# Kernel optimization log

Hardware: AMD Instinct MI355X
Metric: run time of the kernel (lower is better)

## Reference

```python
import jax, jax.numpy as jnp
import numpy as np

B, S, DM, H, HD = 2, 2048, 1024, 16, 64
MEM_SIZE = 1000
K_SIMILAR, K_CONTIG = 8, 2
K_TOTAL = K_SIMILAR + K_CONTIG  # 10 memory tokens
NEG = -1e9


def setup_inputs() -> dict:
    key = jax.random.key(0)
    k1, k2, k3, k4, k5, k6 = jax.random.split(key, 6)
    inputs = jax.random.normal(k1, (B, S, DM), dtype=jnp.float32)
    attention_mask = jnp.ones((B, S), dtype=jnp.float32)
    Wq = jax.random.normal(k2, (DM, H * HD), dtype=jnp.float32) * 0.02
    Wk = jax.random.normal(k3, (DM, H * HD), dtype=jnp.float32) * 0.02
    Wv = jax.random.normal(k4, (DM, H * HD), dtype=jnp.float32) * 0.02
    Wo = jax.random.normal(k5, (H * HD, DM), dtype=jnp.float32) * 0.02
    events = jax.random.normal(k6, (MEM_SIZE, H * HD), dtype=jnp.float32) * 0.02
    return {"inputs": inputs, "attention_mask": attention_mask,
            "Wq": Wq, "Wk": Wk, "Wv": Wv, "Wo": Wo, "events": events}


def _forward(inputs, attention_mask, Wq, Wk, Wv, Wo, events):
    # projections (no bias), split heads: [B, H, S, HD]
    q = (inputs @ Wq).reshape(B, S, H, HD).transpose(0, 2, 1, 3)
    k = (inputs @ Wk).reshape(B, S, H, HD).transpose(0, 2, 1, 3)
    v = (inputs @ Wv).reshape(B, S, H, HD).transpose(0, 2, 1, 3)

    # --- episodic retrieval: cosine top-k of last-token key vs events ---
    qvec = k[:, :, -1, :].reshape(B, H * HD)                       # [B, D]
    qn = qvec / (jnp.linalg.norm(qvec, axis=-1, keepdims=True) + 1e-8)
    en = events / (jnp.linalg.norm(events, axis=-1, keepdims=True) + 1e-8)
    sims = qn @ en.T                                               # [B, M]
    _, topk_idx = jax.lax.top_k(sims, K_TOTAL)                     # [B, K]
    retrieved = events[topk_idx]                                   # [B, K, D]
    retrieved_k = retrieved.reshape(B, K_TOTAL, H, HD).transpose(0, 2, 1, 3)  # [B,H,K,HD]
    retrieved_v = retrieved_k                                      # non-differential path

    aug_k = jnp.concatenate([retrieved_k, k], axis=2)              # [B,H,K+S,HD]
    aug_v = jnp.concatenate([retrieved_v, v], axis=2)

    # --- ALiBi bias: slopes * (pos_i - pos_j) on original cols, 0 on memory cols ---
    slopes = 2.0 ** (-8.0 * jnp.arange(1, H + 1, dtype=jnp.float32) / H)  # [H]
    positions = jnp.arange(S, dtype=jnp.float32)
    pos_diff = positions[:, None] - positions[None, :]             # [S, S]
    alibi = slopes[:, None, None] * pos_diff                       # [H, S, S]
    alibi = jnp.concatenate([jnp.zeros((H, S, K_TOTAL), jnp.float32), alibi], axis=-1)

    # --- causal mask: -1e9 strictly-upper on original cols, 0 on memory cols ---
    tri = jnp.where(jnp.arange(S)[None, :] > jnp.arange(S)[:, None], NEG, 0.0)  # [S,S]
    causal = jnp.concatenate([jnp.zeros((S, K_TOTAL), jnp.float32), tri], axis=-1)

    # --- padding mask: memory tokens always attendable ---
    aug_mask = jnp.concatenate([jnp.ones((B, K_TOTAL), jnp.float32), attention_mask], axis=-1)
    mask_bias = (1.0 - aug_mask)[:, None, None, :] * NEG           # [B,1,1,K+S]

    scores = jnp.einsum("bhqd,bhkd->bhqk", q, aug_k) / np.sqrt(HD)
    scores = scores + alibi[None] + causal[None, None] + mask_bias
    attn = jax.nn.softmax(scores, axis=-1)
    out = jnp.einsum("bhqk,bhkd->bhqd", attn, aug_v)               # [B,H,S,HD]
    out = out.transpose(0, 2, 1, 3).reshape(B, S, H * HD)
    return out @ Wo


def reference(inputs, attention_mask, Wq, Wk, Wv, Wo, events):
    return _forward(inputs, attention_mask, Wq, Wk, Wv, Wo, events)
```

## Files before the change

### kernel.cpp

```cpp
#include <hip/hip_runtime.h>
#include <hip/hip_bf16.h>
#include <math.h>

#define B_   2
#define S_   2048
#define DM_  1024
#define H_   16
#define HD_  64
#define MEM_ 1000
#define KTOT 10
#define NROW (B_ * S_)
#define NEG9 (-1e9f)
#define LDK  72

typedef __attribute__((ext_vector_type(8))) short short8;
typedef __attribute__((ext_vector_type(4))) float f32x4;

__device__ __forceinline__ void gll16(const __hip_bfloat16* g, __hip_bfloat16* l) {
    __builtin_amdgcn_global_load_lds(
        (const __attribute__((address_space(1))) void*)g,
        (__attribute__((address_space(3))) void*)l, 16, 0, 0);
}

__global__ __launch_bounds__(256) void convert_a(const float* __restrict__ in,
                                                 __hip_bfloat16* __restrict__ out) {
    const size_t i = ((size_t)blockIdx.x * 256 + threadIdx.x) * 8;
    float4 a = *(const float4*)&in[i];
    float4 b = *(const float4*)&in[i + 4];
    alignas(16) __hip_bfloat16 t[8];
    t[0] = __float2bfloat16(a.x); t[1] = __float2bfloat16(a.y);
    t[2] = __float2bfloat16(a.z); t[3] = __float2bfloat16(a.w);
    t[4] = __float2bfloat16(b.x); t[5] = __float2bfloat16(b.y);
    t[6] = __float2bfloat16(b.z); t[7] = __float2bfloat16(b.w);
    *(short8*)&out[i] = *(short8*)t;
}

__global__ __launch_bounds__(256) void convert_wT(const float* __restrict__ Wq,
                                                  const float* __restrict__ Wk,
                                                  const float* __restrict__ Wv,
                                                  const float* __restrict__ Wo,
                                                  __hip_bfloat16* __restrict__ Wt) {
    const int g = blockIdx.z;
    const float* W = (g == 0) ? Wq : (g == 1) ? Wk : (g == 2) ? Wv : Wo;
    const int n0 = blockIdx.x * 64, k0 = blockIdx.y * 64;
    __shared__ float T[64][65];
    const int tid = threadIdx.x;
    {
        const int r = tid >> 4, c4 = (tid & 15) * 4;
#pragma unroll
        for (int p = 0; p < 4; ++p) {
            float4 v = *(const float4*)&W[(size_t)(k0 + r + p * 16) * 1024 + n0 + c4];
            T[r + p * 16][c4 + 0] = v.x; T[r + p * 16][c4 + 1] = v.y;
            T[r + p * 16][c4 + 2] = v.z; T[r + p * 16][c4 + 3] = v.w;
        }
    }
    __syncthreads();
    {
        const int n = tid >> 3, off = (tid & 7) * 8;
#pragma unroll
        for (int p = 0; p < 2; ++p) {
            const int nn = n + p * 32;
            alignas(16) __hip_bfloat16 t[8];
#pragma unroll
            for (int j = 0; j < 8; ++j) t[j] = __float2bfloat16(T[off + j][nn]);
            *(short8*)&Wt[((size_t)(g * 1024 + n0 + nn)) * 1024 + k0 + off] = *(short8*)t;
        }
    }
}

__device__ __forceinline__ void store_out(__hip_bfloat16* p, float x) { *p = __float2bfloat16(x); }
__device__ __forceinline__ void store_out(float* p, float x) { *p = x; }

template <typename OutT>
__global__ __launch_bounds__(256) void gemm_mfma(const __hip_bfloat16* __restrict__ A,
                                                 const __hip_bfloat16* __restrict__ Bt,
                                                 OutT* __restrict__ C, int ldc) {
    __shared__ __hip_bfloat16 As[128 * 32];
    __shared__ __hip_bfloat16 Bs[128 * 32];
    const int tid = threadIdx.x;
    const int wave = tid >> 6, lane = tid & 63;
    const int quad = lane >> 4, lm = lane & 15;
    const int wr = wave >> 1, wc = wave & 1;
    const int m0 = blockIdx.y * 128, n0 = blockIdx.x * 128;

    const int r0 = tid >> 2, c0 = (tid & 3) * 8;
    const __hip_bfloat16* ga0 = &A[(size_t)(m0 + r0) * 1024 + c0];
    const __hip_bfloat16* ga1 = &A[(size_t)(m0 + 64 + r0) * 1024 + c0];
    const __hip_bfloat16* gb0 = &Bt[(size_t)(n0 + r0) * 1024 + c0];
    const __hip_bfloat16* gb1 = &Bt[(size_t)(n0 + 64 + r0) * 1024 + c0];
    __hip_bfloat16* la0 = &As[(wave * 64) * 8];
    __hip_bfloat16* la1 = &As[(256 + wave * 64) * 8];
    __hip_bfloat16* lb0 = &Bs[(wave * 64) * 8];
    __hip_bfloat16* lb1 = &Bs[(256 + wave * 64) * 8];

    f32x4 acc[4][4];
#pragma unroll
    for (int i = 0; i < 4; ++i)
#pragma unroll
        for (int j = 0; j < 4; ++j) acc[i][j] = (f32x4){0.f, 0.f, 0.f, 0.f};

    for (int k0 = 0; k0 < 1024; k0 += 32) {
        __syncthreads();
        gll16(ga0 + k0, la0);
        gll16(ga1 + k0, la1);
        gll16(gb0 + k0, lb0);
        gll16(gb1 + k0, lb1);
        __syncthreads();
        short8 af[4], bf4[4];
#pragma unroll
        for (int mt = 0; mt < 4; ++mt)
            af[mt] = *(const short8*)&As[(wr * 64 + mt * 16 + lm) * 32 + quad * 8];
#pragma unroll
        for (int nt = 0; nt < 4; ++nt)
            bf4[nt] = *(const short8*)&Bs[(wc * 64 + nt * 16 + lm) * 32 + quad * 8];
#pragma unroll
        for (int mt = 0; mt < 4; ++mt)
#pragma unroll
            for (int nt = 0; nt < 4; ++nt)
                acc[mt][nt] = __builtin_amdgcn_mfma_f32_16x16x32_bf16(
                    af[mt], bf4[nt], acc[mt][nt], 0, 0, 0);
    }
#pragma unroll
    for (int mt = 0; mt < 4; ++mt)
#pragma unroll
        for (int nt = 0; nt < 4; ++nt) {
            const int col = n0 + wc * 64 + nt * 16 + lm;
#pragma unroll
            for (int i = 0; i < 4; ++i) {
                const int row = m0 + wr * 64 + mt * 16 + quad * 4 + i;
                store_out(&C[(size_t)row * ldc + col], acc[mt][nt][i]);
            }
        }
}

__global__ __launch_bounds__(256) void lastk_kernel(const float* __restrict__ inputs,
                                                    const float* __restrict__ Wk,
                                                    float* __restrict__ lk) {
    const int b = blockIdx.y;
    const int cl = threadIdx.x & 63;
    const int col = blockIdx.x * 64 + cl;
    const int kq = threadIdx.x >> 6;
    __shared__ float xr[1024];
    __shared__ float part[4][64];
    for (int i = threadIdx.x; i < 1024; i += 256)
        xr[i] = inputs[((size_t)(b * S_ + S_ - 1)) * 1024 + i];
    __syncthreads();
    float acc = 0.f;
#pragma unroll 4
    for (int k = kq * 256; k < kq * 256 + 256; ++k)
        acc += xr[k] * Wk[(size_t)k * 1024 + col];
    part[kq][cl] = acc;
    __syncthreads();
    if (threadIdx.x < 64)
        lk[b * 1024 + blockIdx.x * 64 + threadIdx.x] =
            part[0][threadIdx.x] + part[1][threadIdx.x] +
            part[2][threadIdx.x] + part[3][threadIdx.x];
}

__global__ __launch_bounds__(256) void sims_kernel(const float* __restrict__ lk,
                                                   const float* __restrict__ events,
                                                   float* __restrict__ sims) {
    const int b = blockIdx.y;
    const int tid = threadIdx.x;
    const int wave = tid >> 6, lane = tid & 63;
    __shared__ float qv[1024];
    for (int i = tid; i < 1024; i += 256)
        qv[i] = lk[b * 1024 + i];
    __syncthreads();

    const int m = blockIdx.x * 4 + wave;
    if (m >= MEM_) return;
    const float* ev = &events[(size_t)m * 1024];
    float dot = 0.f, nrm = 0.f;
    for (int d = lane; d < 1024; d += 64) {
        float e = ev[d];
        dot += qv[d] * e;
        nrm += e * e;
    }
    for (int off = 32; off; off >>= 1) {
        dot += __shfl_down(dot, off);
        nrm += __shfl_down(nrm, off);
    }
    if (lane == 0) sims[b * 1024 + m] = dot / (sqrtf(nrm) + 1e-8f);
}

__global__ __launch_bounds__(256) void topk10_kernel(const float* __restrict__ sims,
                                                     int* __restrict__ topk) {
    const int b = blockIdx.x;
    const int tid = threadIdx.x;
    __shared__ float sv[1024];
    __shared__ float bv[256];
    __shared__ int   bi[256];
    for (int m = tid; m < 1024; m += 256)
        sv[m] = (m < MEM_) ? sims[b * 1024 + m] : -INFINITY;
    __syncthreads();

    for (int it = 0; it < KTOT; ++it) {
        float best = -INFINITY; int besti = 0x7fffffff;
        for (int m = tid; m < 1024; m += 256) {
            float s = sv[m];
            if (s > best || (s == best && m < besti)) { best = s; besti = m; }
        }
        bv[tid] = best; bi[tid] = besti;
        __syncthreads();
        for (int stride = 128; stride; stride >>= 1) {
            if (tid < stride) {
                float ov = bv[tid + stride]; int oi = bi[tid + stride];
                if (ov > bv[tid] || (ov == bv[tid] && oi < bi[tid])) {
                    bv[tid] = ov; bi[tid] = oi;
                }
            }
            __syncthreads();
        }
        if (tid == 0) { topk[b * KTOT + it] = bi[0]; sv[bi[0]] = -INFINITY; }
        __syncthreads();
    }
}

__global__ __launch_bounds__(256) void attn_mfma(
        const __hip_bfloat16* __restrict__ qkv,
        const float* __restrict__ events,
        const int* __restrict__ topk,
        const float* __restrict__ amask,
        __hip_bfloat16* __restrict__ out) {
    const int b = blockIdx.y >> 4, h = blockIdx.y & 15;
    const int qt = (blockIdx.x + blockIdx.y) & 31;
    const int q0 = qt * 64;
    const int tid = threadIdx.x;
    const int wave = tid >> 6, lane = tid & 63;
    const int quad = lane >> 4, lm = lane & 15;

    const __hip_bfloat16* qf = qkv;
    const __hip_bfloat16* kf = qkv + 1024;
    const __hip_bfloat16* vf = qkv + 2048;

    __shared__ __hip_bfloat16 Qs[64 * LDK];
    __shared__ __hip_bfloat16 Ks[64 * LDK];
    __shared__ __hip_bfloat16 Vt[64 * LDK];
    __shared__ __hip_bfloat16 Ps[64 * LDK];
    __shared__ float colb[64];
    __shared__ float redb[4];

    const float slope = exp2f(-0.5f * (float)(h + 1));

    const int va = tid & 31, vdc = tid >> 5;
    const int vtok0 = va * 2, vd0 = vdc * 8;

    {
        const __hip_bfloat16* src = &qf[((size_t)(b * S_ + q0)) * 3072 + h * 64];
#pragma unroll
        for (int u = 0; u < 2; ++u) {
            int c = tid * 2 + u, row = c >> 3, off = (c & 7) * 8;
            *(short8*)&Qs[row * LDK + off] =
                *(const short8*)&src[(size_t)row * 3072 + off];
        }
    }
    for (int i = tid * 8; i < 64 * LDK; i += 256 * 8)
        *(int4*)&Vt[i] = make_int4(0, 0, 0, 0);
    __syncthreads();
    if (tid < 80) {
        const int tok = tid >> 3, d0 = (tid & 7) * 8;
        const int ev = topk[b * KTOT + tok];
        const float* es = &events[(size_t)ev * 1024 + h * 64 + d0];
#pragma unroll
        for (int j = 0; j < 8; ++j) {
            __hip_bfloat16 x = __float2bfloat16(es[j]);
            Ks[tok * LDK + d0 + j] = x;
            Vt[(d0 + j) * LDK + tok] = x;
        }
    }
    __syncthreads();

    float m_[4], l_[4], mshift[4];
    f32x4 Oa[4];
#pragma unroll
    for (int i = 0; i < 4; ++i) {
        m_[i] = -INFINITY; l_[i] = 0.f;
        mshift[i] = -slope * (float)(q0 + wave * 16 + quad * 4 + i);
    }
#pragma unroll
    for (int nt = 0; nt < 4; ++nt) Oa[nt] = (f32x4){0.f, 0.f, 0.f, 0.f};

    short8 pk[2], pv0, pv1;
    float pam = 1.f;
    auto prefetchKV = [&](int kt) {
        const __hip_bfloat16* ks = &kf[((size_t)(b * S_ + kt * 64)) * 3072 + h * 64];
#pragma unroll
        for (int u = 0; u < 2; ++u) {
            int c = tid * 2 + u, row = c >> 3, off = (c & 7) * 8;
            pk[u] = *(const short8*)&ks[(size_t)row * 3072 + off];
        }
        const __hip_bfloat16* v0 =
            &vf[((size_t)(b * S_ + kt * 64 + vtok0)) * 3072 + h * 64 + vd0];
        pv0 = *(const short8*)v0;
        pv1 = *(const short8*)(v0 + 3072);
        if (tid < 64) pam = amask[b * S_ + kt * 64 + tid];
    };
    auto stageKV = [&](int kt) {
#pragma unroll
        for (int u = 0; u < 2; ++u) {
            int c = tid * 2 + u, row = c >> 3, off = (c & 7) * 8;
            *(short8*)&Ks[row * LDK + off] = pk[u];
        }
#pragma unroll
        for (int j = 0; j < 8; ++j) {
            short2 pr; pr.x = pv0[j]; pr.y = pv1[j];
            *(short2*)&Vt[(vd0 + j) * LDK + vtok0] = pr;
        }
        if (tid < 64)
            colb[tid] = fmaf(-slope, (float)(kt * 64 + tid), (1.f - pam) * NEG9);
    };

    auto qk = [&](f32x4* sa) {
#pragma unroll
        for (int nt = 0; nt < 4; ++nt) sa[nt] = (f32x4){0.f, 0.f, 0.f, 0.f};
#pragma unroll
        for (int ks2 = 0; ks2 < 2; ++ks2) {
            short8 aq = *(const short8*)&Qs[(wave * 16 + lm) * LDK + ks2 * 32 + quad * 8];
#pragma unroll
            for (int nt = 0; nt < 4; ++nt) {
                short8 bk = *(const short8*)&Ks[(nt * 16 + lm) * LDK + ks2 * 32 + quad * 8];
                sa[nt] = __builtin_amdgcn_mfma_f32_16x16x32_bf16(aq, bk, sa[nt], 0, 0, 0);
            }
        }
    };
    auto pv = [&]() {
#pragma unroll
        for (int ks2 = 0; ks2 < 2; ++ks2) {
            short8 ap = *(const short8*)&Ps[(wave * 16 + lm) * LDK + ks2 * 32 + quad * 8];
#pragma unroll
            for (int nt = 0; nt < 4; ++nt) {
                short8 bv = *(const short8*)&Vt[(nt * 16 + lm) * LDK + ks2 * 32 + quad * 8];
                Oa[nt] = __builtin_amdgcn_mfma_f32_16x16x32_bf16(ap, bv, Oa[nt], 0, 0, 0);
            }
        }
    };

    auto softmax_online = [&](const f32x4* sa, int kt, bool diag) {
        float cb[4];
        if (kt >= 0) {
#pragma unroll
            for (int nt = 0; nt < 4; ++nt) cb[nt] = colb[nt * 16 + lm];
        }
#pragma unroll
        for (int i = 0; i < 4; ++i) {
            const int lr = wave * 16 + quad * 4 + i;
            const int rg = q0 + lr;
            float s[4];
#pragma unroll
            for (int nt = 0; nt < 4; ++nt) {
                const int cc = nt * 16 + lm;
                if (kt < 0) {
                    s[nt] = (cc < KTOT) ? fmaf(sa[nt][i], 0.125f, mshift[i]) : NEG9;
                } else {
                    float v = fmaf(sa[nt][i], 0.125f, cb[nt]);
                    s[nt] = (diag && kt * 64 + cc > rg) ? NEG9 : v;
                }
            }
            float rmax = fmaxf(fmaxf(s[0], s[1]), fmaxf(s[2], s[3]));
#pragma unroll
            for (int off = 1; off < 16; off <<= 1)
                rmax = fmaxf(rmax, __shfl_xor(rmax, off, 16));
            const float newm = fmaxf(m_[i], rmax);
            const float al = __expf(m_[i] - newm);
            float p[4], ps = 0.f;
#pragma unroll
            for (int nt = 0; nt < 4; ++nt) {
                p[nt] = __expf(s[nt] - newm);
                ps += p[nt];
            }
#pragma unroll
            for (int off = 1; off < 16; off <<= 1)
                ps += __shfl_xor(ps, off, 16);
            l_[i] = l_[i] * al + ps;
            m_[i] = newm;
#pragma unroll
            for (int nt = 0; nt < 4; ++nt) {
                Oa[nt][i] *= al;
                Ps[lr * LDK + nt * 16 + lm] = __float2bfloat16(p[nt]);
            }
        }
    };

    auto softmax_fast = [&](const f32x4* sa, int cbase, bool diag) {
        float cb[4];
#pragma unroll
        for (int nt = 0; nt < 4; ++nt) cb[nt] = colb[nt * 16 + lm];
#pragma unroll
        for (int i = 0; i < 4; ++i) {
            const int lr = wave * 16 + quad * 4 + i;
            const float cm = m_[i];
            float p[4];
#pragma unroll
            for (int nt = 0; nt < 4; ++nt)
                p[nt] = __expf(fmaf(sa[nt][i], 0.125f, cb[nt]) - cm);
            if (diag) {
                const int rg = q0 + lr;
#pragma unroll
                for (int nt = 0; nt < 4; ++nt)
                    if (cbase + nt * 16 + lm > rg) p[nt] = 0.f;
            }
            float ps = (p[0] + p[1]) + (p[2] + p[3]);
#pragma unroll
            for (int off = 1; off < 16; off <<= 1)
                ps += __shfl_xor(ps, off, 16);
            l_[i] += ps;
#pragma unroll
            for (int nt = 0; nt < 4; ++nt)
                Ps[lr * LDK + nt * 16 + lm] = __float2bfloat16(p[nt]);
        }
    };

    prefetchKV(0);
    {
        f32x4 sa[4];
        qk(sa);
        softmax_online(sa, -1, false);
        pv();
    }
    __syncthreads();
    stageKV(0);
    if (qt >= 1) prefetchKV(1);
    __syncthreads();
    {
        f32x4 sa[4];
        qk(sa);
        softmax_online(sa, 0, qt == 0);
        pv();
    }

    int ktend = 0;
    if (qt >= 1) {
        float mloc = fminf(fminf(m_[0], m_[1]), fminf(m_[2], m_[3]));
#pragma unroll
        for (int off = 1; off < 64; off <<= 1)
            mloc = fminf(mloc, __shfl_xor(mloc, off, 64));
        if (lane == 0) redb[wave] = mloc;
        __syncthreads();
        const float mmin = fminf(fminf(redb[0], redb[1]), fminf(redb[2], redb[3]));
        ktend = min(qt, (int)((118.f - mmin) / (64.f * slope)));
    }
    for (int kt = 1; kt <= ktend; ++kt) {
        __syncthreads();
        stageKV(kt);
        if (kt < ktend) prefetchKV(kt + 1);
        __syncthreads();
        f32x4 sa[4];
        qk(sa);
        softmax_fast(sa, kt * 64, kt == qt);
        pv();
    }

#pragma unroll
    for (int i = 0; i < 4; ++i) {
        const int lr = wave * 16 + quad * 4 + i;
        const float inv = 1.f / l_[i];
        __hip_bfloat16* dst = &out[((size_t)(b * S_ + q0 + lr)) * 1024 + h * 64 + lm];
#pragma unroll
        for (int nt = 0; nt < 4; ++nt)
            dst[nt * 16] = __float2bfloat16(Oa[nt][i] * inv);
    }
}

extern "C" void kernel_launch(void* const* d_in, const int* in_sizes, int n_in,
                              void* d_out, int out_size, void* d_ws, size_t ws_size,
                              hipStream_t stream) {
    const float* inputs = (const float*)d_in[0];
    const float* amask  = (const float*)d_in[1];
    const float* Wq     = (const float*)d_in[2];
    const float* Wk     = (const float*)d_in[3];
    const float* Wv     = (const float*)d_in[4];
    const float* Wo     = (const float*)d_in[5];
    const float* events = (const float*)d_in[6];
    float* out = (float*)d_out;

    __hip_bfloat16* Ax  = (__hip_bfloat16*)d_ws;
    __hip_bfloat16* Wt  = Ax + (size_t)NROW * 1024;
    __hip_bfloat16* qkv = Wt + (size_t)4096 * 1024;
    __hip_bfloat16* ao  = qkv + (size_t)NROW * 3072;
    float* lk   = (float*)(ao + (size_t)NROW * 1024);
    float* sims = lk + 2 * 1024;
    int* topk   = (int*)(sims + 2 * 1024);

    dim3 blk(256);
    convert_a<<<2048, blk, 0, stream>>>(inputs, Ax);
    convert_wT<<<dim3(16, 16, 4), blk, 0, stream>>>(Wq, Wk, Wv, Wo, Wt);
    gemm_mfma<__hip_bfloat16><<<dim3(24, 32), blk, 0, stream>>>(Ax, Wt, qkv, 3072);
    lastk_kernel<<<dim3(16, B_), blk, 0, stream>>>(inputs, Wk, lk);
    sims_kernel<<<dim3(250, B_), blk, 0, stream>>>(lk, events, sims);
    topk10_kernel<<<B_, 256, 0, stream>>>(sims, topk);
    attn_mfma<<<dim3(32, 32), blk, 0, stream>>>(qkv, events, topk, amask, ao);
    gemm_mfma<float><<<dim3(8, 32), blk, 0, stream>>>(
        ao, Wt + (size_t)3072 * 1024, out, 1024);
}
```

Baseline: 269.9 us.

## Merge prep kernels and make attention persistent with atomic work queue

```diff
diff --git a/kernel.cpp b/kernel.cpp
--- a/kernel.cpp
+++ b/kernel.cpp
@@ -12,6 +12,7 @@
 #define NROW (B_ * S_)
 #define NEG9 (-1e9f)
 #define LDK  72
+#define NITEMS 1024
 
 typedef __attribute__((ext_vector_type(8))) short short8;
 typedef __attribute__((ext_vector_type(4))) float f32x4;
@@ -22,49 +23,79 @@
         (__attribute__((address_space(3))) void*)l, 16, 0, 0);
 }
 
-__global__ __launch_bounds__(256) void convert_a(const float* __restrict__ in,
-                                                 __hip_bfloat16* __restrict__ out) {
-    const size_t i = ((size_t)blockIdx.x * 256 + threadIdx.x) * 8;
-    float4 a = *(const float4*)&in[i];
-    float4 b = *(const float4*)&in[i + 4];
-    alignas(16) __hip_bfloat16 t[8];
-    t[0] = __float2bfloat16(a.x); t[1] = __float2bfloat16(a.y);
-    t[2] = __float2bfloat16(a.z); t[3] = __float2bfloat16(a.w);
-    t[4] = __float2bfloat16(b.x); t[5] = __float2bfloat16(b.y);
-    t[6] = __float2bfloat16(b.z); t[7] = __float2bfloat16(b.w);
-    *(short8*)&out[i] = *(short8*)t;
-}
-
-__global__ __launch_bounds__(256) void convert_wT(const float* __restrict__ Wq,
-                                                  const float* __restrict__ Wk,
-                                                  const float* __restrict__ Wv,
-                                                  const float* __restrict__ Wo,
-                                                  __hip_bfloat16* __restrict__ Wt) {
-    const int g = blockIdx.z;
-    const float* W = (g == 0) ? Wq : (g == 1) ? Wk : (g == 2) ? Wv : Wo;
-    const int n0 = blockIdx.x * 64, k0 = blockIdx.y * 64;
-    __shared__ float T[64][65];
-    const int tid = threadIdx.x;
+__global__ __launch_bounds__(256) void prep(const float* __restrict__ inputs,
+                                            const float* __restrict__ Wq,
+                                            const float* __restrict__ Wk,
+                                            const float* __restrict__ Wv,
+                                            const float* __restrict__ Wo,
+                                            __hip_bfloat16* __restrict__ Ax,
+                                            __hip_bfloat16* __restrict__ Wt,
+                                            float* __restrict__ lk,
+                                            int* __restrict__ ctr) {
+    const int bx = blockIdx.x, tid = threadIdx.x;
+    if (bx == 0 && tid == 0) *ctr = 0;
+
+    if (bx < 2048) {
+        const size_t i = ((size_t)bx * 256 + tid) * 8;
+        float4 a = *(const float4*)&inputs[i];
+        float4 b = *(const float4*)&inputs[i + 4];
+        alignas(16) __hip_bfloat16 t[8];
+        t[0] = __float2bfloat16(a.x); t[1] = __float2bfloat16(a.y);
+        t[2] = __float2bfloat16(a.z); t[3] = __float2bfloat16(a.w);
+        t[4] = __float2bfloat16(b.x); t[5] = __float2bfloat16(b.y);
+        t[6] = __float2bfloat16(b.z); t[7] = __float2bfloat16(b.w);
+        *(short8*)&Ax[i] = *(short8*)t;
+        return;
+    }
+    if (bx < 3072) {
+        const int idx = bx - 2048;
+        const int g = idx >> 8, rem = idx & 255;
+        const float* W = (g == 0) ? Wq : (g == 1) ? Wk : (g == 2) ? Wv : Wo;
+        const int n0 = (rem & 15) * 64, k0 = (rem >> 4) * 64;
+        __shared__ float T[64][65];
+        {
+            const int r = tid >> 4, c4 = (tid & 15) * 4;
+#pragma unroll
+            for (int p = 0; p < 4; ++p) {
+                float4 v = *(const float4*)&W[(size_t)(k0 + r + p * 16) * 1024 + n0 + c4];
+                T[r + p * 16][c4 + 0] = v.x; T[r + p * 16][c4 + 1] = v.y;
+                T[r + p * 16][c4 + 2] = v.z; T[r + p * 16][c4 + 3] = v.w;
+            }
+        }
+        __syncthreads();
+        {
+            const int n = tid >> 3, off = (tid & 7) * 8;
+#pragma unroll
+            for (int p = 0; p < 2; ++p) {
+                const int nn = n + p * 32;
+                alignas(16) __hip_bfloat16 t[8];
+#pragma unroll
+                for (int j = 0; j < 8; ++j) t[j] = __float2bfloat16(T[off + j][nn]);
+                *(short8*)&Wt[((size_t)(g * 1024 + n0 + nn)) * 1024 + k0 + off] = *(short8*)t;
+            }
+        }
+        return;
+    }
     {
-        const int r = tid >> 4, c4 = (tid & 15) * 4;
-#pragma unroll
-        for (int p = 0; p < 4; ++p) {
-            float4 v = *(const float4*)&W[(size_t)(k0 + r + p * 16) * 1024 + n0 + c4];
-            T[r + p * 16][c4 + 0] = v.x; T[r + p * 16][c4 + 1] = v.y;
-            T[r + p * 16][c4 + 2] = v.z; T[r + p * 16][c4 + 3] = v.w;
-        }
-    }
-    __syncthreads();
-    {
-        const int n = tid >> 3, off = (tid & 7) * 8;
-#pragma unroll
-        for (int p = 0; p < 2; ++p) {
-            const int nn = n + p * 32;
-            alignas(16) __hip_bfloat16 t[8];
-#pragma unroll
-            for (int j = 0; j < 8; ++j) t[j] = __float2bfloat16(T[off + j][nn]);
-            *(short8*)&Wt[((size_t)(g * 1024 + n0 + nn)) * 1024 + k0 + off] = *(short8*)t;
-        }
+        const int idx = bx - 3072;
+        const int xblk = idx & 15, b = idx >> 4;
+        const int cl = tid & 63;
+        const int col = xblk * 64 + cl;
+        const int kq = tid >> 6;
+        __shared__ float xr[1024];
+        __shared__ float part[4][64];
+        for (int i = tid; i < 1024; i += 256)
+            xr[i] = inputs[((size_t)(b * S_ + S_ - 1)) * 1024 + i];
+        __syncthreads();
+        float acc = 0.f;
+#pragma unroll 4
+        for (int k = kq * 256; k < kq * 256 + 256; ++k)
+            acc += xr[k] * Wk[(size_t)k * 1024 + col];
+        part[kq][cl] = acc;
+        __syncthreads();
+        if (tid < 64)
+            lk[b * 1024 + xblk * 64 + tid] =
+                part[0][tid] + part[1][tid] + part[2][tid] + part[3][tid];
     }
 }
 
@@ -133,30 +164,6 @@
         }
 }
 
-__global__ __launch_bounds__(256) void lastk_kernel(const float* __restrict__ inputs,
-                                                    const float* __restrict__ Wk,
-                                                    float* __restrict__ lk) {
-    const int b = blockIdx.y;
-    const int cl = threadIdx.x & 63;
-    const int col = blockIdx.x * 64 + cl;
-    const int kq = threadIdx.x >> 6;
-    __shared__ float xr[1024];
-    __shared__ float part[4][64];
-    for (int i = threadIdx.x; i < 1024; i += 256)
-        xr[i] = inputs[((size_t)(b * S_ + S_ - 1)) * 1024 + i];
-    __syncthreads();
-    float acc = 0.f;
-#pragma unroll 4
-    for (int k = kq * 256; k < kq * 256 + 256; ++k)
-        acc += xr[k] * Wk[(size_t)k * 1024 + col];
-    part[kq][cl] = acc;
-    __syncthreads();
-    if (threadIdx.x < 64)
-        lk[b * 1024 + blockIdx.x * 64 + threadIdx.x] =
-            part[0][threadIdx.x] + part[1][threadIdx.x] +
-            part[2][threadIdx.x] + part[3][threadIdx.x];
-}
-
 __global__ __launch_bounds__(256) void sims_kernel(const float* __restrict__ lk,
                                                    const float* __restrict__ events,
                                                    float* __restrict__ sims) {
@@ -222,10 +229,8 @@
         const float* __restrict__ events,
         const int* __restrict__ topk,
         const float* __restrict__ amask,
-        __hip_bfloat16* __restrict__ out) {
-    const int b = blockIdx.y >> 4, h = blockIdx.y & 15;
-    const int qt = (blockIdx.x + blockIdx.y) & 31;
-    const int q0 = qt * 64;
+        __hip_bfloat16* __restrict__ out,
+        int* __restrict__ ctr) {
     const int tid = threadIdx.x;
     const int wave = tid >> 6, lane = tid & 63;
     const int quad = lane >> 4, lm = lane & 15;
@@ -240,225 +245,239 @@
     __shared__ __hip_bfloat16 Ps[64 * LDK];
     __shared__ float colb[64];
     __shared__ float redb[4];
-
-    const float slope = exp2f(-0.5f * (float)(h + 1));
+    __shared__ int sItem;
 
     const int va = tid & 31, vdc = tid >> 5;
     const int vtok0 = va * 2, vd0 = vdc * 8;
 
-    {
-        const __hip_bfloat16* src = &qf[((size_t)(b * S_ + q0)) * 3072 + h * 64];
-#pragma unroll
-        for (int u = 0; u < 2; ++u) {
-            int c = tid * 2 + u, row = c >> 3, off = (c & 7) * 8;
-            *(short8*)&Qs[row * LDK + off] =
-                *(const short8*)&src[(size_t)row * 3072 + off];
-        }
-    }
-    for (int i = tid * 8; i < 64 * LDK; i += 256 * 8)
-        *(int4*)&Vt[i] = make_int4(0, 0, 0, 0);
-    __syncthreads();
-    if (tid < 80) {
-        const int tok = tid >> 3, d0 = (tid & 7) * 8;
-        const int ev = topk[b * KTOT + tok];
-        const float* es = &events[(size_t)ev * 1024 + h * 64 + d0];
-#pragma unroll
-        for (int j = 0; j < 8; ++j) {
-            __hip_bfloat16 x = __float2bfloat16(es[j]);
-            Ks[tok * LDK + d0 + j] = x;
-            Vt[(d0 + j) * LDK + tok] = x;
-        }
-    }
-    __syncthreads();
-
-    float m_[4], l_[4], mshift[4];
-    f32x4 Oa[4];
-#pragma unroll
-    for (int i = 0; i < 4; ++i) {
-        m_[i] = -INFINITY; l_[i] = 0.f;
-        mshift[i] = -slope * (float)(q0 + wave * 16 + quad * 4 + i);
-    }
-#pragma unroll
-    for (int nt = 0; nt < 4; ++nt) Oa[nt] = (f32x4){0.f, 0.f, 0.f, 0.f};
-
-    short8 pk[2], pv0, pv1;
-    float pam = 1.f;
-    auto prefetchKV = [&](int kt) {
-        const __hip_bfloat16* ks = &kf[((size_t)(b * S_ + kt * 64)) * 3072 + h * 64];
-#pragma unroll
-        for (int u = 0; u < 2; ++u) {
-            int c = tid * 2 + u, row = c >> 3, off = (c & 7) * 8;
-            pk[u] = *(const short8*)&ks[(size_t)row * 3072 + off];
-        }
-        const __hip_bfloat16* v0 =
-            &vf[((size_t)(b * S_ + kt * 64 + vtok0)) * 3072 + h * 64 + vd0];
-        pv0 = *(const short8*)v0;
-        pv1 = *(const short8*)(v0 + 3072);
-        if (tid < 64) pam = amask[b * S_ + kt * 64 + tid];
-    };
-    auto stageKV = [&](int kt) {
-#pragma unroll
-        for (int u = 0; u < 2; ++u) {
-            int c = tid * 2 + u, row = c >> 3, off = (c & 7) * 8;
-            *(short8*)&Ks[row * LDK + off] = pk[u];
-        }
-#pragma unroll
-        for (int j = 0; j < 8; ++j) {
-            short2 pr; pr.x = pv0[j]; pr.y = pv1[j];
-            *(short2*)&Vt[(vd0 + j) * LDK + vtok0] = pr;
-        }
-        if (tid < 64)
-            colb[tid] = fmaf(-slope, (float)(kt * 64 + tid), (1.f - pam) * NEG9);
-    };
-
-    auto qk = [&](f32x4* sa) {
-#pragma unroll
-        for (int nt = 0; nt < 4; ++nt) sa[nt] = (f32x4){0.f, 0.f, 0.f, 0.f};
-#pragma unroll
-        for (int ks2 = 0; ks2 < 2; ++ks2) {
-            short8 aq = *(const short8*)&Qs[(wave * 16 + lm) * LDK + ks2 * 32 + quad * 8];
-#pragma unroll
-            for (int nt = 0; nt < 4; ++nt) {
-                short8 bk = *(const short8*)&Ks[(nt * 16 + lm) * LDK + ks2 * 32 + quad * 8];
-                sa[nt] = __builtin_amdgcn_mfma_f32_16x16x32_bf16(aq, bk, sa[nt], 0, 0, 0);
-            }
-        }
-    };
-    auto pv = [&]() {
-#pragma unroll
-        for (int ks2 = 0; ks2 < 2; ++ks2) {
-            short8 ap = *(const short8*)&Ps[(wave * 16 + lm) * LDK + ks2 * 32 + quad * 8];
-#pragma unroll
-            for (int nt = 0; nt < 4; ++nt) {
-                short8 bv = *(const short8*)&Vt[(nt * 16 + lm) * LDK + ks2 * 32 + quad * 8];
-                Oa[nt] = __builtin_amdgcn_mfma_f32_16x16x32_bf16(ap, bv, Oa[nt], 0, 0, 0);
-            }
-        }
-    };
-
-    auto softmax_online = [&](const f32x4* sa, int kt, bool diag) {
-        float cb[4];
-        if (kt >= 0) {
+    for (;;) {
+        __syncthreads();
+        if (tid == 0) sItem = atomicAdd(ctr, 1);
+        __syncthreads();
+        const int n = sItem;
+        if (n >= NITEMS) break;
+
+        const int qt = 31 - (n >> 5);
+        const int q0 = qt * 64;
+        const int inner = n & 31;
+        const int h = 15 - ((inner >> 1) & 15);
+        const int b = inner & 1;
+        const float slope = exp2f(-0.5f * (float)(h + 1));
+
+        {
+            const __hip_bfloat16* src = &qf[((size_t)(b * S_ + q0)) * 3072 + h * 64];
+#pragma unroll
+            for (int u = 0; u < 2; ++u) {
+                int c = tid * 2 + u, row = c >> 3, off = (c & 7) * 8;
+                *(short8*)&Qs[row * LDK + off] =
+                    *(const short8*)&src[(size_t)row * 3072 + off];
+            }
+        }
+        for (int i = tid * 8; i < 64 * LDK; i += 256 * 8)
+            *(int4*)&Vt[i] = make_int4(0, 0, 0, 0);
+        __syncthreads();
+        if (tid < 80) {
+            const int tok = tid >> 3, d0 = (tid & 7) * 8;
+            const int ev = topk[b * KTOT + tok];
+            const float* es = &events[(size_t)ev * 1024 + h * 64 + d0];
+#pragma unroll
+            for (int j = 0; j < 8; ++j) {
+                __hip_bfloat16 x = __float2bfloat16(es[j]);
+                Ks[tok * LDK + d0 + j] = x;
+                Vt[(d0 + j) * LDK + tok] = x;
+            }
+        }
+        __syncthreads();
+
+        float m_[4], l_[4], mshift[4];
+        f32x4 Oa[4];
+#pragma unroll
+        for (int i = 0; i < 4; ++i) {
+            m_[i] = -INFINITY; l_[i] = 0.f;
+            mshift[i] = -slope * (float)(q0 + wave * 16 + quad * 4 + i);
+        }
+#pragma unroll
+        for (int nt = 0; nt < 4; ++nt) Oa[nt] = (f32x4){0.f, 0.f, 0.f, 0.f};
+
+        short8 pk[2], pv0, pv1;
+        float pam = 1.f;
+        auto prefetchKV = [&](int kt) {
+            const __hip_bfloat16* ks = &kf[((size_t)(b * S_ + kt * 64)) * 3072 + h * 64];
+#pragma unroll
+            for (int u = 0; u < 2; ++u) {
+                int c = tid * 2 + u, row = c >> 3, off = (c & 7) * 8;
+                pk[u] = *(const short8*)&ks[(size_t)row * 3072 + off];
+            }
+            const __hip_bfloat16* v0 =
+                &vf[((size_t)(b * S_ + kt * 64 + vtok0)) * 3072 + h * 64 + vd0];
+            pv0 = *(const short8*)v0;
+            pv1 = *(const short8*)(v0 + 3072);
+            if (tid < 64) pam = amask[b * S_ + kt * 64 + tid];
+        };
+        auto stageKV = [&](int kt) {
+#pragma unroll
+            for (int u = 0; u < 2; ++u) {
+                int c = tid * 2 + u, row = c >> 3, off = (c & 7) * 8;
+                *(short8*)&Ks[row * LDK + off] = pk[u];
+            }
+#pragma unroll
+            for (int j = 0; j < 8; ++j) {
+                short2 pr; pr.x = pv0[j]; pr.y = pv1[j];
+                *(short2*)&Vt[(vd0 + j) * LDK + vtok0] = pr;
+            }
+            if (tid < 64)
+                colb[tid] = fmaf(-slope, (float)(kt * 64 + tid), (1.f - pam) * NEG9);
+        };
+
+        auto qk = [&](f32x4* sa) {
+#pragma unroll
+            for (int nt = 0; nt < 4; ++nt) sa[nt] = (f32x4){0.f, 0.f, 0.f, 0.f};
+#pragma unroll
+            for (int ks2 = 0; ks2 < 2; ++ks2) {
+                short8 aq = *(const short8*)&Qs[(wave * 16 + lm) * LDK + ks2 * 32 + quad * 8];
+#pragma unroll
+                for (int nt = 0; nt < 4; ++nt) {
+                    short8 bk = *(const short8*)&Ks[(nt * 16 + lm) * LDK + ks2 * 32 + quad * 8];
+                    sa[nt] = __builtin_amdgcn_mfma_f32_16x16x32_bf16(aq, bk, sa[nt], 0, 0, 0);
+                }
+            }
+        };
+        auto pv = [&]() {
+#pragma unroll
+            for (int ks2 = 0; ks2 < 2; ++ks2) {
+                short8 ap = *(const short8*)&Ps[(wave * 16 + lm) * LDK + ks2 * 32 + quad * 8];
+#pragma unroll
+                for (int nt = 0; nt < 4; ++nt) {
+                    short8 bv = *(const short8*)&Vt[(nt * 16 + lm) * LDK + ks2 * 32 + quad * 8];
+                    Oa[nt] = __builtin_amdgcn_mfma_f32_16x16x32_bf16(ap, bv, Oa[nt], 0, 0, 0);
+                }
+            }
+        };
+
+        auto softmax_online = [&](const f32x4* sa, int kt, bool diag) {
+            float cb[4];
+            if (kt >= 0) {
+#pragma unroll
+                for (int nt = 0; nt < 4; ++nt) cb[nt] = colb[nt * 16 + lm];
+            }
+#pragma unroll
+            for (int i = 0; i < 4; ++i) {
+                const int lr = wave * 16 + quad * 4 + i;
+                const int rg = q0 + lr;
+                float s[4];
+#pragma unroll
+                for (int nt = 0; nt < 4; ++nt) {
+                    const int cc = nt * 16 + lm;
+                    if (kt < 0) {
+                        s[nt] = (cc < KTOT) ? fmaf(sa[nt][i], 0.125f, mshift[i]) : NEG9;
+                    } else {
+                        float v = fmaf(sa[nt][i], 0.125f, cb[nt]);
+                        s[nt] = (diag && kt * 64 + cc > rg) ? NEG9 : v;
+                    }
+                }
+                float rmax = fmaxf(fmaxf(s[0], s[1]), fmaxf(s[2], s[3]));
+#pragma unroll
+                for (int off = 1; off < 16; off <<= 1)
+                    rmax = fmaxf(rmax, __shfl_xor(rmax, off, 16));
+                const float newm = fmaxf(m_[i], rmax);
+                const float al = __expf(m_[i] - newm);
+                float p[4], ps = 0.f;
+#pragma unroll
+                for (int nt = 0; nt < 4; ++nt) {
+                    p[nt] = __expf(s[nt] - newm);
+                    ps += p[nt];
+                }
+#pragma unroll
+                for (int off = 1; off < 16; off <<= 1)
+                    ps += __shfl_xor(ps, off, 16);
+                l_[i] = l_[i] * al + ps;
+                m_[i] = newm;
+#pragma unroll
+                for (int nt = 0; nt < 4; ++nt) {
+                    Oa[nt][i] *= al;
+                    Ps[lr * LDK + nt * 16 + lm] = __float2bfloat16(p[nt]);
+                }
+            }
+        };
+
+        auto softmax_fast = [&](const f32x4* sa, int cbase, bool diag) {
+            float cb[4];
 #pragma unroll
             for (int nt = 0; nt < 4; ++nt) cb[nt] = colb[nt * 16 + lm];
-        }
+#pragma unroll
+            for (int i = 0; i < 4; ++i) {
+                const int lr = wave * 16 + quad * 4 + i;
+                const float cm = m_[i];
+                float p[4];
+#pragma unroll
+                for (int nt = 0; nt < 4; ++nt)
+                    p[nt] = __expf(fmaf(sa[nt][i], 0.125f, cb[nt]) - cm);
+                if (diag) {
+                    const int rg = q0 + lr;
+#pragma unroll
+                    for (int nt = 0; nt < 4; ++nt)
+                        if (cbase + nt * 16 + lm > rg) p[nt] = 0.f;
+                }
+                float ps = (p[0] + p[1]) + (p[2] + p[3]);
+#pragma unroll
+                for (int off = 1; off < 16; off <<= 1)
+                    ps += __shfl_xor(ps, off, 16);
+                l_[i] += ps;
+#pragma unroll
+                for (int nt = 0; nt < 4; ++nt)
+                    Ps[lr * LDK + nt * 16 + lm] = __float2bfloat16(p[nt]);
+            }
+        };
+
+        prefetchKV(0);
+        {
+            f32x4 sa[4];
+            qk(sa);
+            softmax_online(sa, -1, false);
+            pv();
+        }
+        __syncthreads();
+        stageKV(0);
+        if (qt >= 1) prefetchKV(1);
+        __syncthreads();
+        {
+            f32x4 sa[4];
+            qk(sa);
+            softmax_online(sa, 0, qt == 0);
+            pv();
+        }
+
+        int ktend = 0;
+        if (qt >= 1) {
+            float mloc = fminf(fminf(m_[0], m_[1]), fminf(m_[2], m_[3]));
+#pragma unroll
+            for (int off = 1; off < 64; off <<= 1)
+                mloc = fminf(mloc, __shfl_xor(mloc, off, 64));
+            if (lane == 0) redb[wave] = mloc;
+            __syncthreads();
+            const float mmin = fminf(fminf(redb[0], redb[1]), fminf(redb[2], redb[3]));
+            ktend = min(qt, (int)((118.f - mmin) / (64.f * slope)));
+        }
+        for (int kt = 1; kt <= ktend; ++kt) {
+            __syncthreads();
+            stageKV(kt);
+            if (kt < ktend) prefetchKV(kt + 1);
+            __syncthreads();
+            f32x4 sa[4];
+            qk(sa);
+            softmax_fast(sa, kt * 64, kt == qt);
+            pv();
+        }
+
 #pragma unroll
         for (int i = 0; i < 4; ++i) {
             const int lr = wave * 16 + quad * 4 + i;
-            const int rg = q0 + lr;
-            float s[4];
-#pragma unroll
-            for (int nt = 0; nt < 4; ++nt) {
-                const int cc = nt * 16 + lm;
-                if (kt < 0) {
-                    s[nt] = (cc < KTOT) ? fmaf(sa[nt][i], 0.125f, mshift[i]) : NEG9;
-                } else {
-                    float v = fmaf(sa[nt][i], 0.125f, cb[nt]);
-                    s[nt] = (diag && kt * 64 + cc > rg) ? NEG9 : v;
-                }
-            }
-            float rmax = fmaxf(fmaxf(s[0], s[1]), fmaxf(s[2], s[3]));
-#pragma unroll
-            for (int off = 1; off < 16; off <<= 1)
-                rmax = fmaxf(rmax, __shfl_xor(rmax, off, 16));
-            const float newm = fmaxf(m_[i], rmax);
-            const float al = __expf(m_[i] - newm);
-            float p[4], ps = 0.f;
-#pragma unroll
-            for (int nt = 0; nt < 4; ++nt) {
-                p[nt] = __expf(s[nt] - newm);
-                ps += p[nt];
-            }
-#pragma unroll
-            for (int off = 1; off < 16; off <<= 1)
-                ps += __shfl_xor(ps, off, 16);
-            l_[i] = l_[i] * al + ps;
-            m_[i] = newm;
-#pragma unroll
-            for (int nt = 0; nt < 4; ++nt) {
-                Oa[nt][i] *= al;
-                Ps[lr * LDK + nt * 16 + lm] = __float2bfloat16(p[nt]);
-            }
-        }
-    };
-
-    auto softmax_fast = [&](const f32x4* sa, int cbase, bool diag) {
-        float cb[4];
-#pragma unroll
-        for (int nt = 0; nt < 4; ++nt) cb[nt] = colb[nt * 16 + lm];
-#pragma unroll
-        for (int i = 0; i < 4; ++i) {
-            const int lr = wave * 16 + quad * 4 + i;
-            const float cm = m_[i];
-            float p[4];
+            const float inv = 1.f / l_[i];
+            __hip_bfloat16* dst = &out[((size_t)(b * S_ + q0 + lr)) * 1024 + h * 64 + lm];
 #pragma unroll
             for (int nt = 0; nt < 4; ++nt)
-                p[nt] = __expf(fmaf(sa[nt][i], 0.125f, cb[nt]) - cm);
-            if (diag) {
-                const int rg = q0 + lr;
-#pragma unroll
-                for (int nt = 0; nt < 4; ++nt)
-                    if (cbase + nt * 16 + lm > rg) p[nt] = 0.f;
-            }
-            float ps = (p[0] + p[1]) + (p[2] + p[3]);
-#pragma unroll
-            for (int off = 1; off < 16; off <<= 1)
-                ps += __shfl_xor(ps, off, 16);
-            l_[i] += ps;
-#pragma unroll
-            for (int nt = 0; nt < 4; ++nt)
-                Ps[lr * LDK + nt * 16 + lm] = __float2bfloat16(p[nt]);
-        }
-    };
-
-    prefetchKV(0);
-    {
-        f32x4 sa[4];
-        qk(sa);
-        softmax_online(sa, -1, false);
-        pv();
-    }
-    __syncthreads();
-    stageKV(0);
-    if (qt >= 1) prefetchKV(1);
-    __syncthreads();
-    {
-        f32x4 sa[4];
-        qk(sa);
-        softmax_online(sa, 0, qt == 0);
-        pv();
-    }
-
-    int ktend = 0;
-    if (qt >= 1) {
-        float mloc = fminf(fminf(m_[0], m_[1]), fminf(m_[2], m_[3]));
-#pragma unroll
-        for (int off = 1; off < 64; off <<= 1)
-            mloc = fminf(mloc, __shfl_xor(mloc, off, 64));
-        if (lane == 0) redb[wave] = mloc;
-        __syncthreads();
-        const float mmin = fminf(fminf(redb[0], redb[1]), fminf(redb[2], redb[3]));
-        ktend = min(qt, (int)((118.f - mmin) / (64.f * slope)));
-    }
-    for (int kt = 1; kt <= ktend; ++kt) {
-        __syncthreads();
-        stageKV(kt);
-        if (kt < ktend) prefetchKV(kt + 1);
-        __syncthreads();
-        f32x4 sa[4];
-        qk(sa);
-        softmax_fast(sa, kt * 64, kt == qt);
-        pv();
-    }
-
-#pragma unroll
-    for (int i = 0; i < 4; ++i) {
-        const int lr = wave * 16 + quad * 4 + i;
-        const float inv = 1.f / l_[i];
-        __hip_bfloat16* dst = &out[((size_t)(b * S_ + q0 + lr)) * 1024 + h * 64 + lm];
-#pragma unroll
-        for (int nt = 0; nt < 4; ++nt)
-            dst[nt * 16] = __float2bfloat16(Oa[nt][i] * inv);
+                dst[nt * 16] = __float2bfloat16(Oa[nt][i] * inv);
+        }
     }
 }
 
@@ -481,15 +500,14 @@
     float* lk   = (float*)(ao + (size_t)NROW * 1024);
     float* sims = lk + 2 * 1024;
     int* topk   = (int*)(sims + 2 * 1024);
+    int* ctr    = topk + B_ * KTOT;
 
     dim3 blk(256);
-    convert_a<<<2048, blk, 0, stream>>>(inputs, Ax);
-    convert_wT<<<dim3(16, 16, 4), blk, 0, stream>>>(Wq, Wk, Wv, Wo, Wt);
-    gemm_mfma<__hip_bfloat16><<<dim3(24, 32), blk, 0, stream>>>(Ax, Wt, qkv, 3072);
-    lastk_kernel<<<dim3(16, B_), blk, 0, stream>>>(inputs, Wk, lk);
+    prep<<<3104, blk, 0, stream>>>(inputs, Wq, Wk, Wv, Wo, Ax, Wt, lk, ctr);
     sims_kernel<<<dim3(250, B_), blk, 0, stream>>>(lk, events, sims);
     topk10_kernel<<<B_, 256, 0, stream>>>(sims, topk);
-    attn_mfma<<<dim3(32, 32), blk, 0, stream>>>(qkv, events, topk, amask, ao);
+    gemm_mfma<__hip_bfloat16><<<dim3(24, 32), blk, 0, stream>>>(Ax, Wt, qkv, 3072);
+    attn_mfma<<<768, blk, 0, stream>>>(qkv, events, topk, amask, ao, ctr);
     gemm_mfma<float><<<dim3(8, 32), blk, 0, stream>>>(
         ao, Wt + (size_t)3072 * 1024, out, 1024);
 }
```

Result: faster. 256.4 us (-5.0%).
